# Performance work log

Measured on AMD Instinct MI355X. Metric: run time of the kernel, lower is better.

## Reference

```python
import jax, jax.numpy as jnp
import numpy as np

B, S, D, H, DH = 4, 2048, 1024, 16, 64
INIT_STD = 0.02
IGNORE = -100000.0


def setup_inputs() -> dict:
    key = jax.random.key(0)
    ks = jax.random.split(key, 5)
    x = jax.random.normal(ks[0], (B, S, D), dtype=jnp.float32)
    W_Q = INIT_STD * jax.random.normal(ks[1], (H, D, DH), dtype=jnp.float32)
    W_K = INIT_STD * jax.random.normal(ks[2], (H, D, DH), dtype=jnp.float32)
    W_V = INIT_STD * jax.random.normal(ks[3], (H, D, DH), dtype=jnp.float32)
    W_O = INIT_STD * jax.random.normal(ks[4], (H, DH, D), dtype=jnp.float32)
    b_Q = jnp.zeros((H, DH), dtype=jnp.float32)
    b_K = jnp.zeros((H, DH), dtype=jnp.float32)
    b_V = jnp.zeros((H, DH), dtype=jnp.float32)
    b_O = jnp.zeros((D,), dtype=jnp.float32)
    return {"x": x, "W_Q": W_Q, "b_Q": b_Q, "W_K": W_K, "b_K": b_K,
            "W_V": W_V, "b_V": b_V, "W_O": W_O, "b_O": b_O}


def reference(x, W_Q, b_Q, W_K, b_K, W_V, b_V, W_O, b_O):
    # x: (B, S, D); projections -> (B, S, H, DH)
    Q = jnp.einsum('bqd,hde->bqhe', x, W_Q) + b_Q
    K = jnp.einsum('bkd,hde->bkhe', x, W_K) + b_K
    V = jnp.einsum('bkd,hde->bkhe', x, W_V) + b_V
    d_head = Q.shape[-1]
    # scores: (B, H, Sq, Sk)
    scores = jnp.einsum('bqhe,bkhe->bhqk', Q, K) / np.sqrt(d_head).astype(np.float32)
    s = scores.shape[-1]
    causal = jnp.triu(jnp.ones((s, s), dtype=bool), k=1)
    scores = jnp.where(causal, jnp.float32(IGNORE), scores)
    A = jax.nn.softmax(scores, axis=-1)
    z = jnp.einsum('bhqk,bkhe->bqhe', A, V)
    # output projection: sum over heads + bias
    attn_out = jnp.einsum('bqhe,hed->bqd', z, W_O) + b_O
    return attn_out
```

## Files before the change

kernel.cpp:

```cpp
#include <hip/hip_runtime.h>


#define B_ 4
#define S_ 2048
#define D_ 1024
#define H_ 16
#define DH_ 64

typedef unsigned short ushort_t;
typedef __attribute__((ext_vector_type(4))) short short4v;
typedef __attribute__((ext_vector_type(8))) short short8v;
typedef __attribute__((ext_vector_type(4))) float floatx4;
typedef __attribute__((ext_vector_type(4))) unsigned short ushort4v;

static __device__ __forceinline__ ushort_t f2bf(float f) {
    union { float f; unsigned u; } v; v.f = f;
    unsigned r = v.u + 0x7fffu + ((v.u >> 16) & 1u);
    return (ushort_t)(r >> 16);
}

static __device__ __forceinline__ float fast_exp2(float x) {
#if __has_builtin(__builtin_amdgcn_exp2f)
    return __builtin_amdgcn_exp2f(x);
#else
    return exp2f(x);
#endif
}

static __device__ __forceinline__ unsigned pack_bf16_tr(float lo, float hi) {
    union { float f; unsigned u; } a, b;
    a.f = lo; b.f = hi;
    return __builtin_amdgcn_perm(b.u, a.u, 0x07060302u);
}

static __device__ __forceinline__ void g2lds16(const void* g, void* l) {
    __builtin_amdgcn_global_load_lds(
        (__attribute__((address_space(1))) void*)(unsigned long long)(size_t)g,
        (__attribute__((address_space(3))) void*)(unsigned int)(size_t)l,
        16, 0, 0);
}

__global__ void prep_kernel(const float* __restrict__ x,
                            const float* __restrict__ wq, const float* __restrict__ wk,
                            const float* __restrict__ wv, const float* __restrict__ wo,
                            ushort_t* __restrict__ xb, ushort_t* __restrict__ wt,
                            ushort_t* __restrict__ wot) {
    __shared__ float tile[32][33];
    int bid = blockIdx.x;
    int tid = threadIdx.x;
    if (bid < 8192) {
        int i = (bid * 256 + tid) * 4;
        float4 v = *(const float4*)&x[i];
        ushort4v o;
        o[0] = f2bf(v.x); o[1] = f2bf(v.y); o[2] = f2bf(v.z); o[3] = f2bf(v.w);
        *(ushort4v*)&xb[i] = o;
        return;
    }
    const float* src;
    ushort_t* d;
    int C, r0, c0;
    if (bid < 11264) {
        int t = bid - 8192;
        int z = t / 64, r = t % 64;
        src = (z < 16 ? wq : (z < 32 ? wk : wv)) + (size_t)(z & 15) * 65536;
        d = wt + (size_t)z * 65536;
        C = 64; r0 = (r >> 1) * 32; c0 = (r & 1) * 32;
    } else {
        int t = bid - 11264;
        int z = t / 64, r = t % 64;
        src = wo + (size_t)z * 65536;
        d = wot + (size_t)z * 64;
        C = 1024; r0 = (r & 1) * 32; c0 = (r >> 1) * 32;
    }
    int tx = tid & 31, ty = tid >> 5;
#pragma unroll
    for (int i = 0; i < 4; ++i)
        tile[ty + i * 8][tx] = src[(size_t)(r0 + ty + i * 8) * C + c0 + tx];
    __syncthreads();
#pragma unroll
    for (int i = 0; i < 4; ++i)
        d[(size_t)(c0 + ty + i * 8) * 1024 + r0 + tx] = f2bf(tile[tx][ty + i * 8]);
}

__global__ __launch_bounds__(256) void gemm_qkv(const ushort_t* __restrict__ A,
                                                const ushort_t* __restrict__ Wt,
                                                const float* __restrict__ bq,
                                                const float* __restrict__ bk,
                                                const float* __restrict__ bv,
                                                ushort_t* __restrict__ Qw,
                                                ushort_t* __restrict__ Kw,
                                                ushort_t* __restrict__ Vw) {
    __shared__ ushort_t sA[128 * 64];
    __shared__ ushort_t sB[128 * 64];
    const int tid = threadIdx.x;
    const int lane = tid & 63, w = tid >> 6;
    const int lq = lane & 15, quad = lane >> 4;
    const int wm = w >> 1, wn = w & 1;
    const int m0 = blockIdx.x * 128, n0 = blockIdx.y * 128;
    const int mat = blockIdx.y >> 3;

    floatx4 acc[4][4] = {};

    for (int k0 = 0; k0 < 1024; k0 += 64) {
        __syncthreads();
#pragma unroll
        for (int p = 0; p < 4; ++p) {
            int rr = w * 32 + p * 8 + (lane >> 3);
            int cc = (lane & 7) ^ (rr & 7);
            g2lds16(&A[(size_t)(m0 + rr) * 1024 + k0 + cc * 8], &sA[(w * 32 + p * 8) * 64]);
            g2lds16(&Wt[(size_t)(n0 + rr) * 1024 + k0 + cc * 8], &sB[(w * 32 + p * 8) * 64]);
        }
        __syncthreads();
#pragma unroll
        for (int ks = 0; ks < 2; ++ks) {
            short8v af[4], bfr[4];
#pragma unroll
            for (int t = 0; t < 4; ++t) {
                int ma = wm * 64 + t * 16 + lq;
                af[t] = *(const short8v*)&sA[ma * 64 + ((((ks << 2) | quad) ^ (ma & 7)) << 3)];
                int nb = wn * 64 + t * 16 + lq;
                bfr[t] = *(const short8v*)&sB[nb * 64 + ((((ks << 2) | quad) ^ (nb & 7)) << 3)];
            }
#pragma unroll
            for (int mt = 0; mt < 4; ++mt)
#pragma unroll
                for (int nt = 0; nt < 4; ++nt)
                    acc[mt][nt] = __builtin_amdgcn_mfma_f32_16x16x32_bf16(af[mt], bfr[nt], acc[mt][nt], 0, 0, 0);
        }
    }

    const float* bias = mat == 0 ? bq : (mat == 1 ? bk : bv);
    float bias_v[4];
#pragma unroll
    for (int nt = 0; nt < 4; ++nt) bias_v[nt] = bias[(n0 & 1023) + wn * 64 + nt * 16 + lq];

#pragma unroll
    for (int mt = 0; mt < 4; ++mt) {
#pragma unroll
        for (int nt = 0; nt < 4; ++nt) {
            int row0 = m0 + wm * 64 + mt * 16 + quad * 4;
            int col = (n0 & 1023) + wn * 64 + nt * 16 + lq;
            int h = col >> 6, e = col & 63;
            if (mat == 2) {
                int b = row0 >> 11, s = row0 & 2047;
                ushort4v pk;
#pragma unroll
                for (int rg = 0; rg < 4; ++rg) pk[rg] = f2bf(acc[mt][nt][rg] + bias_v[nt]);
                *(ushort4v*)&Vw[((size_t)((b << 4) | h) * 64 + e) * 2048 + s] = pk;
            } else {
                ushort_t* Du = mat == 0 ? Qw : Kw;
#pragma unroll
                for (int rg = 0; rg < 4; ++rg) {
                    int row = row0 + rg;
                    int b = row >> 11, s = row & 2047;
                    float v = acc[mt][nt][rg] + bias_v[nt];
                    if (mat == 0) v *= 0.18033688011112042f;
                    Du[((size_t)((b << 4) | h) * 2048 + s) * 64 + e] = f2bf(v);
                }
            }
        }
    }
}

#define VROW 140
__global__ __launch_bounds__(256) void attn_kernel(const ushort_t* __restrict__ Q,
                                                   const ushort_t* __restrict__ Kg,
                                                   const ushort_t* __restrict__ Vt,
                                                   ushort_t* __restrict__ Z) {
    __shared__ ushort_t sK[2][128 * 64];
    __shared__ ushort_t sV[64 * VROW];
    const int tid = threadIdx.x;
    const int lane = tid & 63, w = tid >> 6;
    const int lq = lane & 15, quad = lane >> 4;
    const int bh = blockIdx.x;
    const int b = bh >> 4, h = bh & 15;
    const ushort_t* Qp = Q + (size_t)bh * S_ * DH_;
    const ushort_t* Kp = Kg + (size_t)bh * S_ * DH_;
    const ushort_t* Vp = Vt + (size_t)bh * DH_ * S_;

    const int kbase0 = lq * 64 + ((quad ^ (lq & 7)) << 3);
    const int kbase1 = lq * 64 + (((4 | quad) ^ (lq & 7)) << 3);
    const int vbase = lq * VROW + quad * 4;
    const int vr = w * 16 + (lane >> 2);
    const int vc = (lane & 3) * 32;

    const floatx4 fzero = {0.f, 0.f, 0.f, 0.f};

    auto stageK = [&](int kt, int bs) __attribute__((always_inline)) {
        ushort_t* dK = sK[bs];
#pragma unroll
        for (int p = 0; p < 4; ++p) {
            int rrk = w * 32 + p * 8 + (lane >> 3);
            int ck = (lane & 7) ^ (rrk & 7);
            g2lds16(&Kp[(size_t)(kt * 128 + rrk) * 64 + ck * 8], &dK[(w * 32 + p * 8) * 64]);
        }
    };
    auto loadV = [&](int kt, short8v* vr4) __attribute__((always_inline)) {
        const ushort_t* src = &Vp[(size_t)vr * 2048 + kt * 128 + vc];
#pragma unroll
        for (int j = 0; j < 4; ++j) vr4[j] = *(const short8v*)&src[j * 8];
    };
    auto writeV = [&](const short8v* vr4) __attribute__((always_inline)) {
        ushort_t* dst = &sV[vr * VROW + vc];
#pragma unroll
        for (int j = 0; j < 4; ++j) *(short8v*)&dst[j * 8] = vr4[j];
    };

    for (int pass = 0; pass < 2; ++pass) {
        const int qt = pass == 0 ? (int)blockIdx.y : 15 - (int)blockIdx.y;
        const int q0 = qt * 128;

        short8v qf[2][2];
#pragma unroll
        for (int qi = 0; qi < 2; ++qi)
#pragma unroll
            for (int ks = 0; ks < 2; ++ks)
                qf[qi][ks] = *(const short8v*)&Qp[(size_t)(q0 + w * 32 + qi * 16 + lq) * DH_ + ks * 32 + quad * 8];

        float l_i[2] = {0.f, 0.f};
        floatx4 o[2][4] = {};
        short8v vreg[4];

        stageK(0, 0);
        loadV(0, vreg);

        for (int kt = 0; kt <= qt; ++kt) {
            const bool diag = (kt == qt);
            const ushort_t* cK = sK[kt & 1];

            __syncthreads();
            writeV(vreg);
            if (kt < qt) {
                stageK(kt + 1, (kt + 1) & 1);
                loadV(kt + 1, vreg);
            }

            floatx4 st[8][2];
#pragma unroll
            for (int si = 0; si < 8; ++si) {
                short8v a0 = *(const short8v*)&cK[kbase0 + si * 1024];
                short8v a1 = *(const short8v*)&cK[kbase1 + si * 1024];
#pragma unroll
                for (int qi = 0; qi < 2; ++qi) {
                    st[si][qi] = __builtin_amdgcn_mfma_f32_16x16x32_bf16(a0, qf[qi][0], fzero, 0, 0, 0);
                    st[si][qi] = __builtin_amdgcn_mfma_f32_16x16x32_bf16(a1, qf[qi][1], st[si][qi], 0, 0, 0);
                }
            }

            short4v pf[8][2];
#pragma unroll
            for (int qi = 0; qi < 2; ++qi) {
                const int qg = q0 + w * 32 + qi * 16 + lq;
                float lsum = 0.f;
#pragma unroll
                for (int si = 0; si < 8; ++si) {
                    float p[4];
#pragma unroll
                    for (int rg = 0; rg < 4; ++rg) {
                        float v = st[si][qi][rg];
                        if (diag) {
                            int sg = kt * 128 + si * 16 + quad * 4 + rg;
                            if (sg > qg) v = -1e30f;
                        }
                        p[rg] = fast_exp2(v);
                        lsum += p[rg];
                    }
                    union { unsigned u[2]; short4v v4; } pk;
                    pk.u[0] = pack_bf16_tr(p[0], p[1]);
                    pk.u[1] = pack_bf16_tr(p[2], p[3]);
                    pf[si][qi] = pk.v4;
                }
                l_i[qi] += lsum;
            }

            __syncthreads();

#pragma unroll
            for (int ksp = 0; ksp < 8; ++ksp) {
#pragma unroll
                for (int et = 0; et < 4; ++et) {
                    short4v vf = *(const short4v*)&sV[vbase + et * (16 * VROW) + ksp * 16];
#pragma unroll
                    for (int qi = 0; qi < 2; ++qi)
                        o[qi][et] = __builtin_amdgcn_mfma_f32_16x16x16bf16_1k(pf[ksp][qi], vf, o[qi][et], 0, 0, 0);
                }
            }
        }

#pragma unroll
        for (int qi = 0; qi < 2; ++qi) {
            float lf = l_i[qi];
            lf += __shfl_xor(lf, 16);
            lf += __shfl_xor(lf, 32);
            float linv[4];
#pragma unroll
            for (int rg = 0; rg < 4; ++rg) linv[rg] = 1.0f / __shfl(lf, quad * 4 + rg);
#pragma unroll
            for (int et = 0; et < 4; ++et) {
#pragma unroll
                for (int rg = 0; rg < 4; ++rg) {
                    int qg = q0 + w * 32 + qi * 16 + quad * 4 + rg;
                    int e = et * 16 + lq;
                    Z[((size_t)(b * S_ + qg) * H_ + h) * DH_ + e] = f2bf(o[qi][et][rg] * linv[rg]);
                }
            }
        }
    }
}

__global__ __launch_bounds__(256) void gemm_o(const ushort_t* __restrict__ A,
                                              const ushort_t* __restrict__ Bt,
                                              const float* __restrict__ bias,
                                              float* __restrict__ Dst) {
    __shared__ ushort_t sA[128 * 64];
    __shared__ ushort_t sB[128 * 64];
    const int tid = threadIdx.x;
    const int lane = tid & 63, w = tid >> 6;
    const int lq = lane & 15, quad = lane >> 4;
    const int wm = w >> 1, wn = w & 1;
    const int m0 = blockIdx.x * 128, n0 = blockIdx.y * 128;

    floatx4 acc[4][4] = {};

    for (int k0 = 0; k0 < 1024; k0 += 64) {
        __syncthreads();
#pragma unroll
        for (int p = 0; p < 4; ++p) {
            int rr = w * 32 + p * 8 + (lane >> 3);
            int cc = (lane & 7) ^ (rr & 7);
            g2lds16(&A[(size_t)(m0 + rr) * 1024 + k0 + cc * 8], &sA[(w * 32 + p * 8) * 64]);
            g2lds16(&Bt[(size_t)(n0 + rr) * 1024 + k0 + cc * 8], &sB[(w * 32 + p * 8) * 64]);
        }
        __syncthreads();
#pragma unroll
        for (int ks = 0; ks < 2; ++ks) {
            short8v af[4], bfr[4];
#pragma unroll
            for (int t = 0; t < 4; ++t) {
                int ma = wm * 64 + t * 16 + lq;
                af[t] = *(const short8v*)&sA[ma * 64 + ((((ks << 2) | quad) ^ (ma & 7)) << 3)];
                int nb = wn * 64 + t * 16 + lq;
                bfr[t] = *(const short8v*)&sB[nb * 64 + ((((ks << 2) | quad) ^ (nb & 7)) << 3)];
            }
#pragma unroll
            for (int mt = 0; mt < 4; ++mt)
#pragma unroll
                for (int nt = 0; nt < 4; ++nt)
                    acc[mt][nt] = __builtin_amdgcn_mfma_f32_16x16x32_bf16(af[mt], bfr[nt], acc[mt][nt], 0, 0, 0);
        }
    }

    float bias_v[4];
#pragma unroll
    for (int nt = 0; nt < 4; ++nt) bias_v[nt] = bias[n0 + wn * 64 + nt * 16 + lq];

#pragma unroll
    for (int mt = 0; mt < 4; ++mt) {
#pragma unroll
        for (int nt = 0; nt < 4; ++nt) {
            int row0 = m0 + wm * 64 + mt * 16 + quad * 4;
            int col = n0 + wn * 64 + nt * 16 + lq;
#pragma unroll
            for (int rg = 0; rg < 4; ++rg)
                Dst[(size_t)(row0 + rg) * 1024 + col] = acc[mt][nt][rg] + bias_v[nt];
        }
    }
}

extern "C" void kernel_launch(void* const* d_in, const int* in_sizes, int n_in,
                              void* d_out, int out_size, void* d_ws, size_t ws_size,
                              hipStream_t stream) {
    const float* x  = (const float*)d_in[0];
    const float* wq = (const float*)d_in[1];
    const float* bq = (const float*)d_in[2];
    const float* wk = (const float*)d_in[3];
    const float* bk = (const float*)d_in[4];
    const float* wv = (const float*)d_in[5];
    const float* bv = (const float*)d_in[6];
    const float* wo = (const float*)d_in[7];
    const float* bo = (const float*)d_in[8];

    char* ws = (char*)d_ws;
    size_t off = 0;
    ushort_t* xb  = (ushort_t*)(ws + off); off += (size_t)8192 * 1024 * 2;
    ushort_t* wt  = (ushort_t*)(ws + off); off += (size_t)3 * 1024 * 1024 * 2;
    ushort_t* wot = (ushort_t*)(ws + off); off += (size_t)1024 * 1024 * 2;
    ushort_t* Qw  = (ushort_t*)(ws + off); off += (size_t)8192 * 1024 * 2;
    ushort_t* Kw  = (ushort_t*)(ws + off); off += (size_t)8192 * 1024 * 2;
    ushort_t* Vw  = (ushort_t*)(ws + off); off += (size_t)8192 * 1024 * 2;
    ushort_t* Zw  = (ushort_t*)(ws + off); off += (size_t)8192 * 1024 * 2;

    prep_kernel<<<12288, 256, 0, stream>>>(x, wq, wk, wv, wo, xb, wt, wot);
    gemm_qkv<<<dim3(64, 24), 256, 0, stream>>>(xb, wt, bq, bk, bv, Qw, Kw, Vw);
    attn_kernel<<<dim3(64, 8), 256, 0, stream>>>(Qw, Kw, Vw, Zw);
    gemm_o<<<dim3(64, 8), 256, 0, stream>>>(Zw, wot, bo, (float*)d_out);
}
```

Baseline: 252.8 us.

## Merge paired query tiles into one K/V sweep and vectorize GEMM epilogues

```diff
diff --git a/kernel.cpp b/kernel.cpp
--- a/kernel.cpp
+++ b/kernel.cpp
@@ -99,6 +99,9 @@
     const int m0 = blockIdx.x * 128, n0 = blockIdx.y * 128;
     const int mat = blockIdx.y >> 3;
 
+    const int rsa = (mat == 2 ? wm : wn);
+    const int rsb = (mat == 2 ? wn : wm);
+
     floatx4 acc[4][4] = {};
 
     for (int k0 = 0; k0 < 1024; k0 += 64) {
@@ -116,63 +119,82 @@
             short8v af[4], bfr[4];
 #pragma unroll
             for (int t = 0; t < 4; ++t) {
-                int ma = wm * 64 + t * 16 + lq;
+                int ma = rsa * 64 + t * 16 + lq;
                 af[t] = *(const short8v*)&sA[ma * 64 + ((((ks << 2) | quad) ^ (ma & 7)) << 3)];
-                int nb = wn * 64 + t * 16 + lq;
+                int nb = rsb * 64 + t * 16 + lq;
                 bfr[t] = *(const short8v*)&sB[nb * 64 + ((((ks << 2) | quad) ^ (nb & 7)) << 3)];
             }
-#pragma unroll
-            for (int mt = 0; mt < 4; ++mt)
-#pragma unroll
-                for (int nt = 0; nt < 4; ++nt)
-                    acc[mt][nt] = __builtin_amdgcn_mfma_f32_16x16x32_bf16(af[mt], bfr[nt], acc[mt][nt], 0, 0, 0);
-        }
-    }
-
-    const float* bias = mat == 0 ? bq : (mat == 1 ? bk : bv);
-    float bias_v[4];
-#pragma unroll
-    for (int nt = 0; nt < 4; ++nt) bias_v[nt] = bias[(n0 & 1023) + wn * 64 + nt * 16 + lq];
-
-#pragma unroll
-    for (int mt = 0; mt < 4; ++mt) {
-#pragma unroll
-        for (int nt = 0; nt < 4; ++nt) {
-            int row0 = m0 + wm * 64 + mt * 16 + quad * 4;
-            int col = (n0 & 1023) + wn * 64 + nt * 16 + lq;
-            int h = col >> 6, e = col & 63;
             if (mat == 2) {
+#pragma unroll
+                for (int mt = 0; mt < 4; ++mt)
+#pragma unroll
+                    for (int nt = 0; nt < 4; ++nt)
+                        acc[mt][nt] = __builtin_amdgcn_mfma_f32_16x16x32_bf16(af[mt], bfr[nt], acc[mt][nt], 0, 0, 0);
+            } else {
+#pragma unroll
+                for (int mt = 0; mt < 4; ++mt)
+#pragma unroll
+                    for (int nt = 0; nt < 4; ++nt)
+                        acc[mt][nt] = __builtin_amdgcn_mfma_f32_16x16x32_bf16(bfr[mt], af[nt], acc[mt][nt], 0, 0, 0);
+            }
+        }
+    }
+
+    if (mat == 2) {
+        float bias_v[4];
+#pragma unroll
+        for (int nt = 0; nt < 4; ++nt) bias_v[nt] = bv[(n0 & 1023) + wn * 64 + nt * 16 + lq];
+#pragma unroll
+        for (int mt = 0; mt < 4; ++mt) {
+#pragma unroll
+            for (int nt = 0; nt < 4; ++nt) {
+                int row0 = m0 + wm * 64 + mt * 16 + quad * 4;
+                int col = (n0 & 1023) + wn * 64 + nt * 16 + lq;
                 int b = row0 >> 11, s = row0 & 2047;
+                int h = col >> 6, e = col & 63;
                 ushort4v pk;
 #pragma unroll
                 for (int rg = 0; rg < 4; ++rg) pk[rg] = f2bf(acc[mt][nt][rg] + bias_v[nt]);
                 *(ushort4v*)&Vw[((size_t)((b << 4) | h) * 64 + e) * 2048 + s] = pk;
-            } else {
-                ushort_t* Du = mat == 0 ? Qw : Kw;
-#pragma unroll
-                for (int rg = 0; rg < 4; ++rg) {
-                    int row = row0 + rg;
-                    int b = row >> 11, s = row & 2047;
-                    float v = acc[mt][nt][rg] + bias_v[nt];
-                    if (mat == 0) v *= 0.18033688011112042f;
-                    Du[((size_t)((b << 4) | h) * 2048 + s) * 64 + e] = f2bf(v);
-                }
+            }
+        }
+    } else {
+        ushort_t* Du = mat == 0 ? Qw : Kw;
+        const float* bias = mat == 0 ? bq : bk;
+        const float sc = mat == 0 ? 0.18033688011112042f : 1.0f;
+#pragma unroll
+        for (int mt = 0; mt < 4; ++mt) {
+            int nbase = (n0 & 1023) + wm * 64 + mt * 16 + quad * 4;
+            float4 bvv = *(const float4*)&bias[nbase];
+            float bb[4] = {bvv.x, bvv.y, bvv.z, bvv.w};
+            int h = nbase >> 6, e = nbase & 63;
+#pragma unroll
+            for (int nt = 0; nt < 4; ++nt) {
+                int m = m0 + wn * 64 + nt * 16 + lq;
+                int b = m >> 11, s = m & 2047;
+                ushort4v pk;
+#pragma unroll
+                for (int rg = 0; rg < 4; ++rg) pk[rg] = f2bf((acc[mt][nt][rg] + bb[rg]) * sc);
+                *(ushort4v*)&Du[((size_t)((b << 4) | h) * 2048 + s) * 64 + e] = pk;
             }
         }
     }
 }
 
 #define VROW 140
-__global__ __launch_bounds__(256) void attn_kernel(const ushort_t* __restrict__ Q,
-                                                   const ushort_t* __restrict__ Kg,
-                                                   const ushort_t* __restrict__ Vt,
-                                                   ushort_t* __restrict__ Z) {
+__global__ __launch_bounds__(256, 2) void attn_kernel(const ushort_t* __restrict__ Q,
+                                                      const ushort_t* __restrict__ Kg,
+                                                      const ushort_t* __restrict__ Vt,
+                                                      ushort_t* __restrict__ Z) {
     __shared__ ushort_t sK[2][128 * 64];
     __shared__ ushort_t sV[64 * VROW];
     const int tid = threadIdx.x;
     const int lane = tid & 63, w = tid >> 6;
     const int lq = lane & 15, quad = lane >> 4;
     const int bh = blockIdx.x;
+    const int y = blockIdx.y;
+    const int qtA = y, qtB = 15 - y;
+    const int q0A = qtA * 128, q0B = qtB * 128;
     const int b = bh >> 4, h = bh & 15;
     const ushort_t* Qp = Q + (size_t)bh * S_ * DH_;
     const ushort_t* Kp = Kg + (size_t)bh * S_ * DH_;
@@ -206,58 +228,54 @@
         for (int j = 0; j < 4; ++j) *(short8v*)&dst[j * 8] = vr4[j];
     };
 
-    for (int pass = 0; pass < 2; ++pass) {
-        const int qt = pass == 0 ? (int)blockIdx.y : 15 - (int)blockIdx.y;
-        const int q0 = qt * 128;
-
-        short8v qf[2][2];
-#pragma unroll
-        for (int qi = 0; qi < 2; ++qi)
-#pragma unroll
-            for (int ks = 0; ks < 2; ++ks)
-                qf[qi][ks] = *(const short8v*)&Qp[(size_t)(q0 + w * 32 + qi * 16 + lq) * DH_ + ks * 32 + quad * 8];
-
-        float l_i[2] = {0.f, 0.f};
-        floatx4 o[2][4] = {};
-        short8v vreg[4];
-
-        stageK(0, 0);
-        loadV(0, vreg);
-
-        for (int kt = 0; kt <= qt; ++kt) {
-            const bool diag = (kt == qt);
-            const ushort_t* cK = sK[kt & 1];
-
-            __syncthreads();
-            writeV(vreg);
-            if (kt < qt) {
-                stageK(kt + 1, (kt + 1) & 1);
-                loadV(kt + 1, vreg);
-            }
-
+    short8v qf[4][2];
+#pragma unroll
+    for (int s4 = 0; s4 < 4; ++s4) {
+        int qrow = (s4 < 2 ? q0A : q0B) + w * 32 + (s4 & 1) * 16 + lq;
+#pragma unroll
+        for (int ks = 0; ks < 2; ++ks)
+            qf[s4][ks] = *(const short8v*)&Qp[(size_t)qrow * DH_ + ks * 32 + quad * 8];
+    }
+
+    float l_i[4] = {0.f, 0.f, 0.f, 0.f};
+    floatx4 o[4][4] = {};
+    short8v vreg[4];
+
+    stageK(0, 0);
+    loadV(0, vreg);
+
+    for (int kt = 0; kt <= qtB; ++kt) {
+        const ushort_t* cK = sK[kt & 1];
+
+        __syncthreads();
+        writeV(vreg);
+        if (kt < qtB) {
+            stageK(kt + 1, (kt + 1) & 1);
+            loadV(kt + 1, vreg);
+        }
+
+        auto score = [&](int g, bool diag, int q0, short4v (*pf)[2]) __attribute__((always_inline)) {
             floatx4 st[8][2];
 #pragma unroll
             for (int si = 0; si < 8; ++si) {
                 short8v a0 = *(const short8v*)&cK[kbase0 + si * 1024];
                 short8v a1 = *(const short8v*)&cK[kbase1 + si * 1024];
 #pragma unroll
-                for (int qi = 0; qi < 2; ++qi) {
-                    st[si][qi] = __builtin_amdgcn_mfma_f32_16x16x32_bf16(a0, qf[qi][0], fzero, 0, 0, 0);
-                    st[si][qi] = __builtin_amdgcn_mfma_f32_16x16x32_bf16(a1, qf[qi][1], st[si][qi], 0, 0, 0);
+                for (int j = 0; j < 2; ++j) {
+                    st[si][j] = __builtin_amdgcn_mfma_f32_16x16x32_bf16(a0, qf[g + j][0], fzero, 0, 0, 0);
+                    st[si][j] = __builtin_amdgcn_mfma_f32_16x16x32_bf16(a1, qf[g + j][1], st[si][j], 0, 0, 0);
                 }
             }
-
-            short4v pf[8][2];
-#pragma unroll
-            for (int qi = 0; qi < 2; ++qi) {
-                const int qg = q0 + w * 32 + qi * 16 + lq;
+#pragma unroll
+            for (int j = 0; j < 2; ++j) {
+                const int qg = q0 + w * 32 + j * 16 + lq;
                 float lsum = 0.f;
 #pragma unroll
                 for (int si = 0; si < 8; ++si) {
                     float p[4];
 #pragma unroll
                     for (int rg = 0; rg < 4; ++rg) {
-                        float v = st[si][qi][rg];
+                        float v = st[si][j][rg];
                         if (diag) {
                             int sg = kt * 128 + si * 16 + quad * 4 + rg;
                             if (sg > qg) v = -1e30f;
@@ -268,41 +286,51 @@
                     union { unsigned u[2]; short4v v4; } pk;
                     pk.u[0] = pack_bf16_tr(p[0], p[1]);
                     pk.u[1] = pack_bf16_tr(p[2], p[3]);
-                    pf[si][qi] = pk.v4;
+                    pf[si][j] = pk.v4;
                 }
-                l_i[qi] += lsum;
-            }
-
-            __syncthreads();
-
+                l_i[g + j] += lsum;
+            }
+        };
+        auto pv = [&](int g, const short4v (*pf)[2]) __attribute__((always_inline)) {
 #pragma unroll
             for (int ksp = 0; ksp < 8; ++ksp) {
 #pragma unroll
                 for (int et = 0; et < 4; ++et) {
                     short4v vf = *(const short4v*)&sV[vbase + et * (16 * VROW) + ksp * 16];
 #pragma unroll
-                    for (int qi = 0; qi < 2; ++qi)
-                        o[qi][et] = __builtin_amdgcn_mfma_f32_16x16x16bf16_1k(pf[ksp][qi], vf, o[qi][et], 0, 0, 0);
+                    for (int j = 0; j < 2; ++j)
+                        o[g + j][et] = __builtin_amdgcn_mfma_f32_16x16x16bf16_1k(pf[ksp][j], vf, o[g + j][et], 0, 0, 0);
                 }
             }
-        }
-
-#pragma unroll
-        for (int qi = 0; qi < 2; ++qi) {
-            float lf = l_i[qi];
-            lf += __shfl_xor(lf, 16);
-            lf += __shfl_xor(lf, 32);
-            float linv[4];
-#pragma unroll
-            for (int rg = 0; rg < 4; ++rg) linv[rg] = 1.0f / __shfl(lf, quad * 4 + rg);
-#pragma unroll
-            for (int et = 0; et < 4; ++et) {
-#pragma unroll
-                for (int rg = 0; rg < 4; ++rg) {
-                    int qg = q0 + w * 32 + qi * 16 + quad * 4 + rg;
-                    int e = et * 16 + lq;
-                    Z[((size_t)(b * S_ + qg) * H_ + h) * DH_ + e] = f2bf(o[qi][et][rg] * linv[rg]);
-                }
+        };
+
+        short4v pfB[8][2];
+        score(2, kt == qtB, q0B, pfB);
+        __syncthreads();
+        pv(2, pfB);
+        if (kt <= qtA) {
+            short4v pfA[8][2];
+            score(0, kt == qtA, q0A, pfA);
+            pv(0, pfA);
+        }
+    }
+
+#pragma unroll
+    for (int s4 = 0; s4 < 4; ++s4) {
+        float lf = l_i[s4];
+        lf += __shfl_xor(lf, 16);
+        lf += __shfl_xor(lf, 32);
+        float linv[4];
+#pragma unroll
+        for (int rg = 0; rg < 4; ++rg) linv[rg] = 1.0f / __shfl(lf, quad * 4 + rg);
+        int q0 = (s4 < 2 ? q0A : q0B) + w * 32 + (s4 & 1) * 16;
+#pragma unroll
+        for (int et = 0; et < 4; ++et) {
+#pragma unroll
+            for (int rg = 0; rg < 4; ++rg) {
+                int qg = q0 + quad * 4 + rg;
+                int e = et * 16 + lq;
+                Z[((size_t)(b * S_ + qg) * H_ + h) * DH_ + e] = f2bf(o[s4][et][rg] * linv[rg]);
             }
         }
     }
@@ -337,32 +365,33 @@
             short8v af[4], bfr[4];
 #pragma unroll
             for (int t = 0; t < 4; ++t) {
-                int ma = wm * 64 + t * 16 + lq;
+                int ma = wn * 64 + t * 16 + lq;
                 af[t] = *(const short8v*)&sA[ma * 64 + ((((ks << 2) | quad) ^ (ma & 7)) << 3)];
-                int nb = wn * 64 + t * 16 + lq;
+                int nb = wm * 64 + t * 16 + lq;
                 bfr[t] = *(const short8v*)&sB[nb * 64 + ((((ks << 2) | quad) ^ (nb & 7)) << 3)];
             }
 #pragma unroll
             for (int mt = 0; mt < 4; ++mt)
 #pragma unroll
                 for (int nt = 0; nt < 4; ++nt)
-                    acc[mt][nt] = __builtin_amdgcn_mfma_f32_16x16x32_bf16(af[mt], bfr[nt], acc[mt][nt], 0, 0, 0);
-        }
-    }
-
-    float bias_v[4];
-#pragma unroll
-    for (int nt = 0; nt < 4; ++nt) bias_v[nt] = bias[n0 + wn * 64 + nt * 16 + lq];
+                    acc[mt][nt] = __builtin_amdgcn_mfma_f32_16x16x32_bf16(bfr[mt], af[nt], acc[mt][nt], 0, 0, 0);
+        }
+    }
 
 #pragma unroll
     for (int mt = 0; mt < 4; ++mt) {
+        int nbase = n0 + wm * 64 + mt * 16 + quad * 4;
+        float4 bvv = *(const float4*)&bias[nbase];
+        float bb[4] = {bvv.x, bvv.y, bvv.z, bvv.w};
 #pragma unroll
         for (int nt = 0; nt < 4; ++nt) {
-            int row0 = m0 + wm * 64 + mt * 16 + quad * 4;
-            int col = n0 + wn * 64 + nt * 16 + lq;
-#pragma unroll
-            for (int rg = 0; rg < 4; ++rg)
-                Dst[(size_t)(row0 + rg) * 1024 + col] = acc[mt][nt][rg] + bias_v[nt];
+            int m = m0 + wn * 64 + nt * 16 + lq;
+            float4 ov;
+            ov.x = acc[mt][nt][0] + bb[0];
+            ov.y = acc[mt][nt][1] + bb[1];
+            ov.z = acc[mt][nt][2] + bb[2];
+            ov.w = acc[mt][nt][3] + bb[3];
+            *(float4*)&Dst[(size_t)m * 1024 + nbase] = ov;
         }
     }
 }
```

After: 405.8 us. 60.5% more time.
